# Optimization experiments

Hardware: AMD Instinct MI355X
Metric: run time of the kernel (lower is better)

The kernel has to match this reference:

```python
import jax, jax.numpy as jnp
import numpy as np

L_SIDE = 32
N_PIX = 12 * L_SIDE * L_SIDE      # 12288 sphere pixels
N_VALID = N_PIX // 2              # theta <= pi/2 hemisphere (first half by construction)
A_TH, B_TH, C_TH = 0.03, 1.0, 1.0  # ellipsoid semi-axes (thickness, 1, 1)


def _sphere_angles(n):
    # Deterministic Fibonacci-lattice sphere sampling standing in for SphereHealpix.
    i = np.arange(n, dtype=np.float64)
    z = 1.0 - 2.0 * (i + 0.5) / n          # cos(theta), descending -> theta<=pi/2 iff i < n/2
    theta = np.arccos(z)
    phi = (i * np.pi * (3.0 - np.sqrt(5.0))) % (2.0 * np.pi)
    return theta.astype(np.float32), phi.astype(np.float32)


def _ellipse_valid():
    # Faithful translation of ReconstructionModel.ellipse_valid for the valid hemisphere.
    theta_all, phi_all = _sphere_angles(N_PIX)
    tv = theta_all[:N_VALID].astype(np.float32)
    pv = phi_all[:N_VALID].astype(np.float32)
    a, b, c = np.float32(A_TH), np.float32(B_TH), np.float32(C_TH)
    # cartesian coords of valid pixels (computed BEFORE the angle shift)
    xv = np.cos(pv) * np.sin(tv)
    yv = np.sin(pv) * np.sin(tv)
    # meshgrid(phi, x) / meshgrid(theta, y) with ij indexing -> angles vary on rows, coords on cols
    phi = ((pv + np.pi / 2) % (2 * np.pi)).astype(np.float32)[:, None]   # [Nv,1]
    theta = ((tv + np.pi / 2) % np.pi).astype(np.float32)[:, None]       # [Nv,1]
    x = xv[None, :]
    y = yv[None, :]
    x_c = np.sin(2 * theta) / 2 * np.cos(phi)
    y_c = -np.sin(2 * theta) / 2 * np.sin(phi)
    z_c = (np.cos(2 * theta) + 1) / 2
    r = np.sqrt(2 * (np.cos(2 * theta) + 1)) / 2 + np.float32(1e-5)
    a2, b2, c2 = a * a, b * b, c * c
    ct, st = np.cos(theta), np.sin(theta)
    cp, sp = np.cos(phi), np.sin(phi)
    ct2, ct4 = ct ** 2, ct ** 4
    cp2 = cp ** 2
    x2, y2 = x ** 2, y ** 2
    s2p = np.sin(2.0 * phi)
    with np.errstate(invalid='ignore'):
        S = (-b2 * ct2 + b2 * ct4 - b2 * y2 - c2 * x2
             + a2 * b2 * ct4 + b2 * c2 * ct2 - b2 * c2 * ct4
             - b2 * x2 * cp2 + b2 * y2 * cp2 + c2 * x2 * cp2 - c2 * y2 * cp2
             - a2 * x2 * ct2 + c2 * x2 * ct2
             + b2 * x * y * s2p - c2 * x * y * s2p
             + a2 * x2 * cp2 * ct2 - a2 * y2 * cp2 * ct2
             - c2 * x2 * cp2 * ct2 + c2 * y2 * cp2 * ct2
             + 2.0 * b2 * x * cp * ct * st - 2.0 * b2 * y * ct * sp * st
             + 2.0 * c2 * x * y * cp * ct2 * sp - 2.0 * a2 * x * y * cp * ct2 * sp)
        num = (a * c * np.sqrt(S)
               - a2 * b * ct2 + 2.0 * a2 * b * ct4
               + 2.0 * b * c2 * ct2 - 2.0 * b * c2 * ct4
               + a2 * b * x * cp * ct * st - b * c2 * x * cp * ct * st
               - a2 * b * y * ct * sp * st + b * c2 * y * ct * sp * st)
        den = b * (a2 * ct2 - c2 * ct2 + c2)
        z = num / den
        f = ((x - x_c) ** 2 + (y - y_c) ** 2 + (z - z_c) ** 2) / r ** 2
    f = np.where(np.isnan(f), np.float32(0.0), f)   # f[f != f] = 0
    return f.astype(np.float32)


def setup_inputs() -> dict:
    key = jax.random.key(0)
    x = jax.random.uniform(key, (8, 16, N_PIX), dtype=jnp.float32)
    all_responses = jnp.asarray(_ellipse_valid())   # [N_VALID, N_VALID]
    return {"x": x, "all_responses": all_responses}


def reference(x, all_responses):
    nv = all_responses.shape[0]
    # masked gather: theta <= pi/2 is exactly the first nv pixels by construction
    x_valid = x[:, :, :nv]                                   # [B,C,Nv]
    mixture = jnp.einsum('bcn,nm->bcm', x_valid, all_responses)
    mixture = jnp.clip(mixture, 0.0, 1.0)                    # mix='clip'
    # masked scatter back into zero buffer
    out = jnp.zeros_like(x).at[:, :, :nv].set(mixture)
    return out
```

## Files before the change

kernel.cpp:

```cpp
#include <hip/hip_runtime.h>
#include <hip/hip_bf16.h>


#define NPIX 12288
#define NV   6144
#define MR   128
#define KST  128
#define LDK  6208
#define LDA  6208
#define LDP  6208
#define PARTF ((size_t)MR * LDP)

typedef __attribute__((ext_vector_type(8))) short bf16x8;
typedef __attribute__((ext_vector_type(4))) float f32x4;
typedef __attribute__((ext_vector_type(4))) unsigned u32x4;

__device__ __forceinline__ unsigned pk2(float lo, float hi) {
    __hip_bfloat162 h = __float22bfloat162_rn(make_float2(lo, hi));
    union { __hip_bfloat162 h; unsigned u; } v; v.h = h; return v.u;
}

__device__ __forceinline__ void gld16(const void* g, void* l) {
    __builtin_amdgcn_global_load_lds(
        (const __attribute__((address_space(1))) void*)g,
        (__attribute__((address_space(3))) void*)l, 16, 0, 0);
}

__global__ __launch_bounds__(256) void prep_kernel(const float* __restrict__ x,
                                                   unsigned short* __restrict__ abf) {
    int q = blockIdx.x * 256 + threadIdx.x;
    int m = q / (NV / 8);
    int r = q % (NV / 8);
    int k = r * 8;
    const float* src = x + (size_t)m * NPIX + k;
    f32x4 a = *(const f32x4*)(src);
    f32x4 b = *(const f32x4*)(src + 4);
    u32x4 o;
    o[0] = pk2(a[0], a[1]); o[1] = pk2(a[2], a[3]);
    o[2] = pk2(b[0], b[1]); o[3] = pk2(b[2], b[3]);
    *(u32x4*)(abf + (size_t)m * LDA + k) = o;
}

__global__ __launch_bounds__(256) void trans_kernel(const float* __restrict__ R,
                                                    unsigned short* __restrict__ RT) {
    const int tid = threadIdx.x;
    const int w = tid >> 6, l = tid & 63;
    const int band = blockIdx.x % 192;
    const int nc   = blockIdx.x / 192;
    const int k0 = band * 32 + w * 8;
    const int n0 = nc * 256 + l * 4;
    const float* src = R + (size_t)k0 * NV + n0;
    f32x4 r[8];
    #pragma unroll
    for (int j = 0; j < 8; ++j) r[j] = *(const f32x4*)(src + (size_t)j * NV);
    #pragma unroll
    for (int c = 0; c < 4; ++c) {
        u32x4 o;
        o[0] = pk2(r[0][c], r[1][c]);
        o[1] = pk2(r[2][c], r[3][c]);
        o[2] = pk2(r[4][c], r[5][c]);
        o[3] = pk2(r[6][c], r[7][c]);
        *(u32x4*)(RT + (size_t)(n0 + c) * LDK + k0) = o;
    }
}

__global__ __launch_bounds__(256) void gemm2_kernel(
        const unsigned short* __restrict__ A,
        const unsigned short* __restrict__ RT,
        float* __restrict__ wpart) {
    __shared__ unsigned char Bs[2][16384];

    const int tid = threadIdx.x;
    const int w = tid >> 6, l = tid & 63;
    const int ln = l & 15, lg = l >> 4;
    const int chunk = blockIdx.x & 7;
    const int nb = blockIdx.x >> 3;
    const int n0 = nb * 64;
    const int kbase = chunk * 768;
    const int nsi = 768 / KST;

    int fo[4], nn[4];
    const char* gg[4];
    #pragma unroll
    for (int i = 0; i < 4; ++i) {
        fo[i] = tid * 16 + i * 4096;
        nn[i] = fo[i] >> 8;
        const int ko = (fo[i] & 255) ^ ((nn[i] & 7) << 4);
        gg[i] = (const char*)(RT + (size_t)(n0 + nn[i]) * LDK + kbase) + ko;
    }

    size_t arow0 = (size_t)(w * 32 + ln) * LDA + kbase + lg * 8;
    size_t arow1 = arow0 + (size_t)16 * LDA;

    f32x4 acc[2][4];
    #pragma unroll
    for (int a = 0; a < 2; ++a)
        #pragma unroll
        for (int b = 0; b < 4; ++b) {
            acc[a][b][0] = 0.f; acc[a][b][1] = 0.f;
            acc[a][b][2] = 0.f; acc[a][b][3] = 0.f;
        }

    #pragma unroll
    for (int i = 0; i < 4; ++i) gld16(gg[i], &Bs[0][fo[i]]);
    __syncthreads();

    const int swn = (ln & 7) << 4;
    #pragma unroll 1
    for (int t = 0; t < nsi; ++t) {
        if (t + 1 < nsi) {
            const int nb2 = (t + 1) & 1;
            #pragma unroll
            for (int i = 0; i < 4; ++i) gld16(gg[i] + (t + 1) * 256, &Bs[nb2][fo[i]]);
        }
        const unsigned char* buf = Bs[t & 1];
        bf16x8 afr[2][4];
        #pragma unroll
        for (int ks = 0; ks < 4; ++ks) {
            afr[0][ks] = *(const bf16x8*)(A + arow0 + ks * 32);
            afr[1][ks] = *(const bf16x8*)(A + arow1 + ks * 32);
        }
        #pragma unroll
        for (int nt = 0; nt < 4; ++nt) {
            const int rowb = (nt * 16 + ln) * 256;
            #pragma unroll
            for (int ks = 0; ks < 4; ++ks) {
                bf16x8 bfr = *(const bf16x8*)(buf + rowb + (((lg * 16) + ks * 64) ^ swn));
                acc[0][nt] = __builtin_amdgcn_mfma_f32_16x16x32_bf16(afr[0][ks], bfr, acc[0][nt], 0, 0, 0);
                acc[1][nt] = __builtin_amdgcn_mfma_f32_16x16x32_bf16(afr[1][ks], bfr, acc[1][nt], 0, 0, 0);
            }
        }
        arow0 += KST; arow1 += KST;
        __syncthreads();
    }

    float* dst = wpart + (size_t)chunk * PARTF;
    #pragma unroll
    for (int mt = 0; mt < 2; ++mt) {
        const int mbase = w * 32 + mt * 16 + lg * 4;
        #pragma unroll
        for (int nt = 0; nt < 4; ++nt) {
            const size_t cb = (size_t)(n0 + nt * 16 + ln);
            #pragma unroll
            for (int j = 0; j < 4; ++j)
                dst[(size_t)(mbase + j) * LDP + cb] = acc[mt][nt][j];
        }
    }
}

__global__ __launch_bounds__(256) void reduce_kernel(float* __restrict__ out,
        const float* __restrict__ wpart) {
    int q = blockIdx.x * 256 + threadIdx.x;
    int m = q / (NV / 4);
    int r = q % (NV / 4);
    f32x4 a;
    a[0] = 0.f; a[1] = 0.f; a[2] = 0.f; a[3] = 0.f;
    #pragma unroll 1
    for (int p = 0; p < 8; ++p) {
        f32x4 c = *(const f32x4*)(wpart + (size_t)p * PARTF + (size_t)m * LDP + r * 4);
        #pragma unroll
        for (int i = 0; i < 4; ++i) a[i] += c[i];
    }
    f32x4 cz, z;
    #pragma unroll
    for (int i = 0; i < 4; ++i) {
        cz[i] = fminf(fmaxf(a[i], 0.f), 1.f);
        z[i] = 0.f;
    }
    size_t base = (size_t)m * NPIX + r * 4;
    *(f32x4*)(out + base) = cz;
    *(f32x4*)(out + base + NV) = z;
}

typedef float2 fl2;
__device__ __forceinline__ bf16x8 cvt8(f32x4 a, f32x4 b) {
    union { unsigned u[4]; bf16x8 v; } r;
    r.u[0] = pk2(a[0], a[1]); r.u[1] = pk2(a[2], a[3]);
    r.u[2] = pk2(b[0], b[1]); r.u[3] = pk2(b[2], b[3]);
    return r.v;
}
__device__ __forceinline__ void sload(const float*& bptr, fl2 (&r)[8]) {
    #pragma unroll
    for (int gi = 0; gi < 4; ++gi) {
        const float* p = bptr + (size_t)(gi * 32) * NV;
        r[2 * gi]     = *(const fl2*)(p);
        r[2 * gi + 1] = *(const fl2*)(p + NV);
    }
    bptr += (size_t)KST * NV;
}
__device__ __forceinline__ void wstage(unsigned char* buf, const fl2 (&r)[8],
                                       int kq, int nq, int sw0, int sw1) {
    #pragma unroll
    for (int gi = 0; gi < 4; ++gi) {
        unsigned lo = pk2(r[2 * gi].x, r[2 * gi + 1].x);
        unsigned hi = pk2(r[2 * gi].y, r[2 * gi + 1].y);
        const int kbyte = (kq + gi * 32) * 2;
        *(unsigned*)(buf + nq * 256       + (kbyte ^ sw0)) = lo;
        *(unsigned*)(buf + (nq + 1) * 256 + (kbyte ^ sw1)) = hi;
    }
}
__device__ __forceinline__ void compute_fb(const unsigned char* buf,
        const float* __restrict__ X, size_t arow0, size_t arow1,
        int ln, int lg, f32x4 (&acc)[2][2]) {
    bf16x8 afr[2][4];
    #pragma unroll
    for (int ks = 0; ks < 4; ++ks) {
        f32x4 p0 = *(const f32x4*)(X + arow0 + ks * 32);
        f32x4 p1 = *(const f32x4*)(X + arow0 + ks * 32 + 4);
        afr[0][ks] = cvt8(p0, p1);
        f32x4 q0 = *(const f32x4*)(X + arow1 + ks * 32);
        f32x4 q1 = *(const f32x4*)(X + arow1 + ks * 32 + 4);
        afr[1][ks] = cvt8(q0, q1);
    }
    const int swn = (ln & 7) << 4;
    #pragma unroll
    for (int nt = 0; nt < 2; ++nt) {
        const int rowb = (nt * 16 + ln) * 256;
        #pragma unroll
        for (int ks = 0; ks < 4; ++ks) {
            bf16x8 bfr = *(const bf16x8*)(buf + rowb + (((lg * 16) + ks * 64) ^ swn));
            acc[0][nt] = __builtin_amdgcn_mfma_f32_16x16x32_bf16(afr[0][ks], bfr, acc[0][nt], 0, 0, 0);
            acc[1][nt] = __builtin_amdgcn_mfma_f32_16x16x32_bf16(afr[1][ks], bfr, acc[1][nt], 0, 0, 0);
        }
    }
}
__global__ __launch_bounds__(256) void gemm_fb_kernel(const float* __restrict__ X,
        const float* __restrict__ R, float* __restrict__ out) {
    __shared__ unsigned char Bs0[32 * 256];
    __shared__ unsigned char Bs1[32 * 256];
    const int tid = threadIdx.x;
    const int w = tid >> 6, l = tid & 63;
    const int ln = l & 15, lg = l >> 4;
    const int chunk = blockIdx.x / 192;
    const int nb = blockIdx.x % 192;
    const int n0 = nb * 32;
    const int kbase = chunk * (NV / 2);
    const int nsi = (NV / 2) / KST;
    const int kq = (tid >> 4) * 2;
    const int nq = (tid & 15) * 2;
    const float* bptr = R + (size_t)(kbase + kq) * NV + (n0 + nq);
    const int sw0 = (nq & 7) << 4;
    const int sw1 = ((nq + 1) & 7) << 4;
    size_t arow0 = (size_t)(w * 32 + ln) * NPIX + kbase + lg * 8;
    size_t arow1 = arow0 + (size_t)16 * NPIX;
    f32x4 acc[2][2];
    #pragma unroll
    for (int a = 0; a < 2; ++a)
        #pragma unroll
        for (int b = 0; b < 2; ++b) {
            acc[a][b][0] = 0.f; acc[a][b][1] = 0.f;
            acc[a][b][2] = 0.f; acc[a][b][3] = 0.f;
        }
    fl2 ring0[8], ring1[8];
    sload(bptr, ring0);
    sload(bptr, ring1);
    wstage(Bs0, ring0, kq, nq, sw0, sw1);
    __syncthreads();
    #pragma unroll 1
    for (int it = 0; it < nsi / 2; ++it) {
        const int s = it * 2;
        if (s + 2 < nsi) sload(bptr, ring0);
        compute_fb(Bs0, X, arow0, arow1, ln, lg, acc);
        arow0 += KST; arow1 += KST;
        wstage(Bs1, ring1, kq, nq, sw0, sw1);
        __syncthreads();
        if (s + 3 < nsi) sload(bptr, ring1);
        compute_fb(Bs1, X, arow0, arow1, ln, lg, acc);
        arow0 += KST; arow1 += KST;
        if (s + 2 < nsi) wstage(Bs0, ring0, kq, nq, sw0, sw1);
        __syncthreads();
    }
    float* dst = out + (size_t)chunk * NV;
    #pragma unroll
    for (int mt = 0; mt < 2; ++mt) {
        const int mbase = w * 32 + mt * 16 + lg * 4;
        #pragma unroll
        for (int nt = 0; nt < 2; ++nt) {
            const size_t cb = (size_t)(n0 + nt * 16 + ln);
            #pragma unroll
            for (int j = 0; j < 4; ++j)
                dst[(size_t)(mbase + j) * NPIX + cb] = acc[mt][nt][j];
        }
    }
}
__global__ __launch_bounds__(256) void reduce_fb_kernel(float* __restrict__ out) {
    int q = blockIdx.x * 256 + threadIdx.x;
    int m = q / (NV / 4);
    int r = q % (NV / 4);
    size_t base = (size_t)m * NPIX + r * 4;
    f32x4 a = *(f32x4*)(out + base);
    f32x4 b = *(f32x4*)(out + base + NV);
    f32x4 cz, z;
    #pragma unroll
    for (int i = 0; i < 4; ++i) {
        float v = a[i] + b[i];
        cz[i] = fminf(fmaxf(v, 0.f), 1.f);
        z[i] = 0.f;
    }
    *(f32x4*)(out + base) = cz;
    *(f32x4*)(out + base + NV) = z;
}

extern "C" void kernel_launch(void* const* d_in, const int* in_sizes, int n_in,
                              void* d_out, int out_size, void* d_ws, size_t ws_size,
                              hipStream_t stream) {
    const float* x = (const float*)d_in[0];
    const float* R = (const float*)d_in[1];
    float* out = (float*)d_out;

    const size_t abytes  = (size_t)MR * LDA * 2;
    const size_t rtbytes = (size_t)NV * LDK * 2;
    const size_t wbytes  = 8 * PARTF * 4;

    if (ws_size >= abytes + rtbytes + wbytes) {
        unsigned short* abf = (unsigned short*)d_ws;
        unsigned short* rt  = (unsigned short*)((char*)d_ws + abytes);
        float* wpart = (float*)((char*)d_ws + abytes + rtbytes);
        prep_kernel<<<(MR * NV / 8) / 256, 256, 0, stream>>>(x, abf);
        trans_kernel<<<192 * 24, 256, 0, stream>>>(R, rt);
        gemm2_kernel<<<96 * 8, 256, 0, stream>>>(abf, rt, wpart);
        reduce_kernel<<<(MR * NV / 4) / 256, 256, 0, stream>>>(out, wpart);
    } else {
        gemm_fb_kernel<<<192 * 2, 256, 0, stream>>>(x, R, out);
        reduce_fb_kernel<<<(MR * NV / 4) / 256, 256, 0, stream>>>(out);
    }
}
```

Measured before the change: 292.9 us.

## Fuse R transpose and bf16 conversion into the GEMM via register-staged LDS

Removes the separate transpose kernel that wrote a bf16 transposed copy of the response matrix to workspace. The GEMM now loads fp32 R tiles directly into registers, converts and transposes them into swizzled LDS buffers, and double-buffers with a two-stage register ring. This eliminates one kernel launch and a full round trip of the 6144x6144 matrix through global memory. In exchange the GEMM reads fp32 (twice the bytes) and spends more VALU and register pressure on conversion instead of using async global-to-LDS loads.

```diff
diff --git a/kernel.cpp b/kernel.cpp
--- a/kernel.cpp
+++ b/kernel.cpp
@@ -6,7 +6,6 @@
 #define NV   6144
 #define MR   128
 #define KST  128
-#define LDK  6208
 #define LDA  6208
 #define LDP  6208
 #define PARTF ((size_t)MR * LDP)
@@ -18,12 +17,6 @@
 __device__ __forceinline__ unsigned pk2(float lo, float hi) {
     __hip_bfloat162 h = __float22bfloat162_rn(make_float2(lo, hi));
     union { __hip_bfloat162 h; unsigned u; } v; v.h = h; return v.u;
-}
-
-__device__ __forceinline__ void gld16(const void* g, void* l) {
-    __builtin_amdgcn_global_load_lds(
-        (const __attribute__((address_space(1))) void*)g,
-        (__attribute__((address_space(3))) void*)l, 16, 0, 0);
 }
 
 __global__ __launch_bounds__(256) void prep_kernel(const float* __restrict__ x,
@@ -41,53 +34,67 @@
     *(u32x4*)(abf + (size_t)m * LDA + k) = o;
 }
 
-__global__ __launch_bounds__(256) void trans_kernel(const float* __restrict__ R,
-                                                    unsigned short* __restrict__ RT) {
-    const int tid = threadIdx.x;
-    const int w = tid >> 6, l = tid & 63;
-    const int band = blockIdx.x % 192;
-    const int nc   = blockIdx.x / 192;
-    const int k0 = band * 32 + w * 8;
-    const int n0 = nc * 256 + l * 4;
-    const float* src = R + (size_t)k0 * NV + n0;
-    f32x4 r[8];
-    #pragma unroll
-    for (int j = 0; j < 8; ++j) r[j] = *(const f32x4*)(src + (size_t)j * NV);
+__device__ __forceinline__ void sload3(const float*& rp, f32x4 (&r)[8]) {
+    #pragma unroll
+    for (int j = 0; j < 8; ++j) r[j] = *(const f32x4*)(rp + (size_t)j * NV);
+    rp += (size_t)KST * NV;
+}
+
+__device__ __forceinline__ void wstage3(unsigned char* buf, const f32x4 (&r)[8],
+                                        int q, int kb) {
     #pragma unroll
     for (int c = 0; c < 4; ++c) {
+        const int n_loc = q * 4 + c;
         u32x4 o;
         o[0] = pk2(r[0][c], r[1][c]);
         o[1] = pk2(r[2][c], r[3][c]);
         o[2] = pk2(r[4][c], r[5][c]);
         o[3] = pk2(r[6][c], r[7][c]);
-        *(u32x4*)(RT + (size_t)(n0 + c) * LDK + k0) = o;
-    }
-}
-
-__global__ __launch_bounds__(256) void gemm2_kernel(
+        *(u32x4*)(buf + n_loc * 256 + (kb ^ ((n_loc & 7) << 4))) = o;
+    }
+}
+
+__device__ __forceinline__ void compute3(const unsigned char* buf,
         const unsigned short* __restrict__ A,
-        const unsigned short* __restrict__ RT,
+        size_t arow0, size_t arow1, int ln, int lg, f32x4 (&acc)[2][4]) {
+    bf16x8 afr[2][4];
+    #pragma unroll
+    for (int ks = 0; ks < 4; ++ks) {
+        afr[0][ks] = *(const bf16x8*)(A + arow0 + ks * 32);
+        afr[1][ks] = *(const bf16x8*)(A + arow1 + ks * 32);
+    }
+    const int swn = (ln & 7) << 4;
+    #pragma unroll
+    for (int nt = 0; nt < 4; ++nt) {
+        const int rowb = (nt * 16 + ln) * 256;
+        #pragma unroll
+        for (int ks = 0; ks < 4; ++ks) {
+            bf16x8 bfr = *(const bf16x8*)(buf + rowb + (((lg * 16) + ks * 64) ^ swn));
+            acc[0][nt] = __builtin_amdgcn_mfma_f32_16x16x32_bf16(afr[0][ks], bfr, acc[0][nt], 0, 0, 0);
+            acc[1][nt] = __builtin_amdgcn_mfma_f32_16x16x32_bf16(afr[1][ks], bfr, acc[1][nt], 0, 0, 0);
+        }
+    }
+}
+
+__global__ __launch_bounds__(256) void gemm3_kernel(
+        const unsigned short* __restrict__ A,
+        const float* __restrict__ R,
         float* __restrict__ wpart) {
-    __shared__ unsigned char Bs[2][16384];
+    __shared__ __align__(64) unsigned char Bs0[16384];
+    __shared__ __align__(64) unsigned char Bs1[16384];
 
     const int tid = threadIdx.x;
     const int w = tid >> 6, l = tid & 63;
     const int ln = l & 15, lg = l >> 4;
+    const int q = ln;
     const int chunk = blockIdx.x & 7;
     const int nb = blockIdx.x >> 3;
     const int n0 = nb * 64;
     const int kbase = chunk * 768;
     const int nsi = 768 / KST;
-
-    int fo[4], nn[4];
-    const char* gg[4];
-    #pragma unroll
-    for (int i = 0; i < 4; ++i) {
-        fo[i] = tid * 16 + i * 4096;
-        nn[i] = fo[i] >> 8;
-        const int ko = (fo[i] & 255) ^ ((nn[i] & 7) << 4);
-        gg[i] = (const char*)(RT + (size_t)(n0 + nn[i]) * LDK + kbase) + ko;
-    }
+    const int kb = w * 64 + lg * 16;
+
+    const float* rp = R + (size_t)(kbase + w * 32 + lg * 8) * NV + n0 + q * 4;
 
     size_t arow0 = (size_t)(w * 32 + ln) * LDA + kbase + lg * 8;
     size_t arow1 = arow0 + (size_t)16 * LDA;
@@ -101,36 +108,24 @@
             acc[a][b][2] = 0.f; acc[a][b][3] = 0.f;
         }
 
-    #pragma unroll
-    for (int i = 0; i < 4; ++i) gld16(gg[i], &Bs[0][fo[i]]);
+    f32x4 ring0[8], ring1[8];
+    sload3(rp, ring0);
+    sload3(rp, ring1);
+    wstage3(Bs0, ring0, q, kb);
     __syncthreads();
 
-    const int swn = (ln & 7) << 4;
     #pragma unroll 1
-    for (int t = 0; t < nsi; ++t) {
-        if (t + 1 < nsi) {
-            const int nb2 = (t + 1) & 1;
-            #pragma unroll
-            for (int i = 0; i < 4; ++i) gld16(gg[i] + (t + 1) * 256, &Bs[nb2][fo[i]]);
-        }
-        const unsigned char* buf = Bs[t & 1];
-        bf16x8 afr[2][4];
-        #pragma unroll
-        for (int ks = 0; ks < 4; ++ks) {
-            afr[0][ks] = *(const bf16x8*)(A + arow0 + ks * 32);
-            afr[1][ks] = *(const bf16x8*)(A + arow1 + ks * 32);
-        }
-        #pragma unroll
-        for (int nt = 0; nt < 4; ++nt) {
-            const int rowb = (nt * 16 + ln) * 256;
-            #pragma unroll
-            for (int ks = 0; ks < 4; ++ks) {
-                bf16x8 bfr = *(const bf16x8*)(buf + rowb + (((lg * 16) + ks * 64) ^ swn));
-                acc[0][nt] = __builtin_amdgcn_mfma_f32_16x16x32_bf16(afr[0][ks], bfr, acc[0][nt], 0, 0, 0);
-                acc[1][nt] = __builtin_amdgcn_mfma_f32_16x16x32_bf16(afr[1][ks], bfr, acc[1][nt], 0, 0, 0);
-            }
-        }
+    for (int it = 0; it < nsi / 2; ++it) {
+        const int s = it * 2;
+        if (s + 2 < nsi) sload3(rp, ring0);
+        compute3(Bs0, A, arow0, arow1, ln, lg, acc);
         arow0 += KST; arow1 += KST;
+        wstage3(Bs1, ring1, q, kb);
+        __syncthreads();
+        if (s + 3 < nsi) sload3(rp, ring1);
+        compute3(Bs1, A, arow0, arow1, ln, lg, acc);
+        arow0 += KST; arow1 += KST;
+        if (s + 2 < nsi) wstage3(Bs0, ring0, q, kb);
         __syncthreads();
     }
 
@@ -308,17 +303,14 @@
     const float* R = (const float*)d_in[1];
     float* out = (float*)d_out;
 
-    const size_t abytes  = (size_t)MR * LDA * 2;
-    const size_t rtbytes = (size_t)NV * LDK * 2;
-    const size_t wbytes  = 8 * PARTF * 4;
-
-    if (ws_size >= abytes + rtbytes + wbytes) {
+    const size_t abytes = (size_t)MR * LDA * 2;
+    const size_t wbytes = 8 * PARTF * 4;
+
+    if (ws_size >= abytes + wbytes) {
         unsigned short* abf = (unsigned short*)d_ws;
-        unsigned short* rt  = (unsigned short*)((char*)d_ws + abytes);
-        float* wpart = (float*)((char*)d_ws + abytes + rtbytes);
+        float* wpart = (float*)((char*)d_ws + abytes);
         prep_kernel<<<(MR * NV / 8) / 256, 256, 0, stream>>>(x, abf);
-        trans_kernel<<<192 * 24, 256, 0, stream>>>(R, rt);
-        gemm2_kernel<<<96 * 8, 256, 0, stream>>>(abf, rt, wpart);
+        gemm3_kernel<<<96 * 8, 256, 0, stream>>>(abf, R, wpart);
         reduce_kernel<<<(MR * NV / 4) / 256, 256, 0, stream>>>(out, wpart);
     } else {
         gemm_fb_kernel<<<192 * 2, 256, 0, stream>>>(x, R, out);
```

Measured after the change: 236.3 us. -19.3%, faster.
